# Kernel tuning notes

Hardware: AMD Instinct MI355X
Metric: run time of the kernel (lower is better)

## Reference

```python
import jax, jax.numpy as jnp
import numpy as np

V = 50000   # vocab
E = 512     # embedding_dim
H = 512     # hidden_dim
HD = 256    # hidden per direction = H // 2
L = 2       # num_layers
B = 64      # batch
T = 256     # sequence_length
K = 7       # tagset size
START, STOP = 5, 6
NEG = -10000.0


def setup_inputs() -> dict:
    key = jax.random.key(0)
    ks = jax.random.split(key, 12)
    sentence = jax.random.randint(ks[0], (T, B), 0, V)          # [T, B] token ids
    emb = jax.random.normal(ks[1], (V, E), jnp.float32) * 0.02  # embedding table
    # PyTorch LSTM params, stacked: [layer, direction, ...]; gate order i,f,g,o
    w_ih = jax.random.normal(ks[2], (L, 2, 4 * HD, E), jnp.float32) * 0.05
    w_hh = jax.random.normal(ks[3], (L, 2, 4 * HD, HD), jnp.float32) * 0.05
    b_ih = jax.random.normal(ks[4], (L, 2, 4 * HD), jnp.float32) * 0.05
    b_hh = jax.random.normal(ks[5], (L, 2, 4 * HD), jnp.float32) * 0.05
    w_out = jax.random.normal(ks[6], (K, H), jnp.float32) * 0.05  # hidden2tag
    b_out = jax.random.normal(ks[7], (K,), jnp.float32) * 0.05
    trans = jax.random.normal(ks[8], (K, K), jnp.float32)
    trans = trans.at[START, :].set(NEG).at[:, STOP].set(NEG)      # CRF transitions[next, prev]
    h0 = jax.random.normal(ks[9], (2 * L, B, HD), jnp.float32)    # random init hidden, as in module
    c0 = jax.random.normal(ks[10], (2 * L, B, HD), jnp.float32)
    return dict(sentence=sentence, emb=emb, w_ih=w_ih, w_hh=w_hh, b_ih=b_ih,
                b_hh=b_hh, w_out=w_out, b_out=b_out, trans=trans, h0=h0, c0=c0)


def _lstm_dir(x, w_ih_d, w_hh_d, b_ih_d, b_hh_d, h0_d, c0_d, reverse):
    # x: [T, B, in]; returns hidden sequence [T, B, HD]
    xg = jnp.einsum('tbe,ge->tbg', x, w_ih_d) + b_ih_d + b_hh_d  # precompute input gates

    def step(carry, g_t):
        h, c = carry
        g = g_t + h @ w_hh_d.T
        i, f, gg, o = jnp.split(g, 4, axis=-1)
        i = jax.nn.sigmoid(i); f = jax.nn.sigmoid(f)
        gg = jnp.tanh(gg);     o = jax.nn.sigmoid(o)
        c = f * c + i * gg
        h = o * jnp.tanh(c)
        return (h, c), h

    _, hs = jax.lax.scan(step, (h0_d, c0_d), xg, reverse=reverse)
    return hs


def _bilstm_feats(sentence, emb, w_ih, w_hh, b_ih, b_hh, w_out, b_out, h0, c0):
    x = emb[sentence]  # [T, B, E]
    for l in range(L):
        hf = _lstm_dir(x, w_ih[l, 0], w_hh[l, 0], b_ih[l, 0], b_hh[l, 0], h0[2 * l], c0[2 * l], False)
        hb = _lstm_dir(x, w_ih[l, 1], w_hh[l, 1], b_ih[l, 1], b_hh[l, 1], h0[2 * l + 1], c0[2 * l + 1], True)
        x = jnp.concatenate([hf, hb], axis=-1)  # [T, B, H]
    return x @ w_out.T + b_out  # [T, B, K]


def _viterbi(feats, trans):
    # feats: [T, B, K]; vectorized over batch (original looped per sequence)
    v0 = jnp.full((B, K), NEG, feats.dtype).at[:, START].set(0.0)

    def step(v, feat_t):
        sc = v[:, None, :] + trans[None, :, :]   # [B, next, prev]
        bp = jnp.argmax(sc, axis=2)              # [B, K]
        v2 = jnp.max(sc, axis=2) + feat_t
        return v2, bp

    v, bps = jax.lax.scan(step, v0, feats)       # bps: [T, B, K]
    term = v + trans[STOP][None, :]
    last = jnp.argmax(term, axis=1)              # [B]
    score = jnp.max(term, axis=1)                # [B] path score

    def back(tag, bp_t):
        prev = jnp.take_along_axis(bp_t, tag[:, None], axis=1)[:, 0]
        return prev, tag

    _, path = jax.lax.scan(back, last, bps, reverse=True)  # [T, B]
    return path.T.astype(jnp.int32), score


def reference(sentence, emb, w_ih, w_hh, b_ih, b_hh, w_out, b_out, trans, h0, c0):
    feats = _bilstm_feats(sentence, emb, w_ih, w_hh, b_ih, b_hh, w_out, b_out, h0, c0)
    best_path, path_score = _viterbi(feats, trans)
    return best_path, path_score
```

## Files before the change

kernel.cpp:

```cpp
#include <hip/hip_runtime.h>
#include <stdint.h>

#define T_LEN 256
#define BATCH 64
#define EDIM  512
#define HDIM  256
#define GDIM  1024
#define KTAG  7
#define NEGV  -10000.0f

using u16 = unsigned short;
using u32 = unsigned int;
using u64 = unsigned long long;

typedef short    bf16x8 __attribute__((ext_vector_type(8)));
typedef float    f32x4  __attribute__((ext_vector_type(4)));

__device__ __forceinline__ float bflo(u32 u) { return __uint_as_float(u << 16); }
__device__ __forceinline__ float bfhi(u32 u) { return __uint_as_float(u & 0xffff0000u); }
__device__ __forceinline__ float bf2f(u16 u) { return __uint_as_float(((u32)u) << 16); }
__device__ __forceinline__ u16 f2bf(float f) {
    u32 x = __float_as_uint(f);
    u32 r = x + 0x7fffu + ((x >> 16) & 1u);
    return (u16)(r >> 16);
}
__device__ __forceinline__ u32 pack2(float a, float b) {
    return (u32)f2bf(a) | ((u32)f2bf(b) << 16);
}
__device__ __forceinline__ float fsig(float x)  { return __builtin_amdgcn_rcpf(1.f + __expf(-x)); }
__device__ __forceinline__ float ftanh(float x) { return 1.f - 2.f * __builtin_amdgcn_rcpf(1.f + __expf(2.f * x)); }

__device__ __forceinline__ int dot4i8(int a, int b, int c) {
#if __has_builtin(__builtin_amdgcn_sdot4)
    return __builtin_amdgcn_sdot4(a, b, c, false);
#else
    c += (int)(signed char)(a & 0xff)         * (int)(signed char)(b & 0xff);
    c += (int)(signed char)((a >> 8) & 0xff)  * (int)(signed char)((b >> 8) & 0xff);
    c += (int)(signed char)((a >> 16) & 0xff) * (int)(signed char)((b >> 16) & 0xff);
    c += (int)(signed char)(a >> 24)          * (int)(signed char)(b >> 24);
    return c;
#endif
}

__device__ __forceinline__ void bar_lds() {
    asm volatile("s_waitcnt lgkmcnt(0)" ::: "memory");
    __builtin_amdgcn_s_barrier();
    asm volatile("" ::: "memory");
}

__device__ __forceinline__ void gload_lds16(const void* g, void* l) {
    __builtin_amdgcn_global_load_lds((const __attribute__((address_space(1))) u32*)g,
                                     (__attribute__((address_space(3))) u32*)l, 16, 0, 0);
}

__global__ __launch_bounds__(64) void embed_k(const int* __restrict__ sent,
                                              const float* __restrict__ emb,
                                              u16* __restrict__ X) {
    int tb = blockIdx.x;
    int tok = sent[tb];
    const float4* src = (const float4*)(emb + (size_t)tok * EDIM);
    float4 a = src[threadIdx.x * 2];
    float4 b = src[threadIdx.x * 2 + 1];
    uint4 o;
    o.x = pack2(a.x, a.y); o.y = pack2(a.z, a.w);
    o.z = pack2(b.x, b.y); o.w = pack2(b.z, b.w);
    ((uint4*)(X + (size_t)tb * EDIM))[threadIdx.x] = o;
}

__global__ __launch_bounds__(256) void conv_wih(const float* __restrict__ W,
                                                u16* __restrict__ WB) {
    int g = blockIdx.x * 256 + threadIdx.x;
    const float4* src = (const float4*)(W + (size_t)g * 8);
    float4 a = src[0], b = src[1];
    uint4 o;
    o.x = pack2(a.x, a.y); o.y = pack2(a.z, a.w);
    o.z = pack2(b.x, b.y); o.w = pack2(b.z, b.w);
    *(uint4*)(WB + (size_t)g * 8) = o;
}

__global__ __launch_bounds__(256) void repack_whh_i8(const float* __restrict__ Whh,
                                                     uint4* __restrict__ WQ,
                                                     float* __restrict__ SCL) {
    int g  = blockIdx.x * 256 + threadIdx.x;
    int ld = g >> 10, row = g & 1023;
    const float* src = Whh + ((size_t)ld * GDIM + row) * HDIM;
    float m = 1e-30f;
    for (int k4 = 0; k4 < 64; ++k4) {
        float4 w = ((const float4*)src)[k4];
        m = fmaxf(m, fmaxf(fmaxf(fabsf(w.x), fabsf(w.y)), fmaxf(fabsf(w.z), fabsf(w.w))));
    }
    float inv = 127.f / m;
    SCL[ld * GDIM + row] = m / 127.f;
    int r = row >> 8, j = row & 255;
    for (int c8 = 0; c8 < 16; ++c8) {
        u32 dw[4];
        #pragma unroll
        for (int d4 = 0; d4 < 4; ++d4) {
            u32 p = 0;
            #pragma unroll
            for (int bb = 0; bb < 4; ++bb) {
                float w = src[c8 * 16 + d4 * 4 + bb];
                int q = (int)rintf(w * inv);
                q = q > 127 ? 127 : (q < -127 ? -127 : q);
                p |= ((u32)(q & 0xff)) << (8 * bb);
            }
            dw[d4] = p;
        }
        WQ[(size_t)(((ld * 4 + r) * 16 + c8) * 256 + j)] =
            (uint4){dw[0], dw[1], dw[2], dw[3]};
    }
}

__global__ __launch_bounds__(256) void gemm_xg(const u16* __restrict__ A,
                                               const u16* __restrict__ W,
                                               const float* __restrict__ Bih,
                                               const float* __restrict__ Bhh,
                                               u16* __restrict__ XG) {
    const int d    = blockIdx.z;
    const int brow = blockIdx.x;
    const int bcol = blockIdx.y;
    const int tid  = threadIdx.x;
    const int lane = tid & 63;
    const int wv   = tid >> 6;
    const int l15  = lane & 15;
    const int quad = lane >> 4;
    const int wr   = wv >> 1, wc = wv & 1;

    __shared__ u16 As[128 * 64];
    __shared__ u16 Bs[128 * 64];

    const u16* Wd = W + (size_t)d * GDIM * EDIM;
    const int srow = tid >> 3;
    const int scol = (tid & 7) * 8;
    const u16* ga = A  + (size_t)(brow * 128 + srow) * EDIM + scol;
    const u16* gb = Wd + (size_t)(bcol * 128 + srow) * EDIM + scol;
    u16* la = As + srow * 64 + scol;
    u16* lb = Bs + srow * 64 + scol;

    f32x4 acc[4][4];
    #pragma unroll
    for (int mt = 0; mt < 4; ++mt)
        #pragma unroll
        for (int nt = 0; nt < 4; ++nt)
            acc[mt][nt] = (f32x4){0.f, 0.f, 0.f, 0.f};

    for (int k0 = 0; k0 < EDIM; k0 += 64) {
        #pragma unroll
        for (int it = 0; it < 4; ++it) {
            gload_lds16(ga + (size_t)(it * 32) * EDIM + k0, la + it * 32 * 64);
            gload_lds16(gb + (size_t)(it * 32) * EDIM + k0, lb + it * 32 * 64);
        }
        __syncthreads();
        #pragma unroll
        for (int ks = 0; ks < 2; ++ks) {
            bf16x8 av[4], bv[4];
            #pragma unroll
            for (int mt = 0; mt < 4; ++mt)
                av[mt] = *(const bf16x8*)(As + (wr * 64 + mt * 16 + l15) * 64 + ks * 32 + quad * 8);
            #pragma unroll
            for (int nt = 0; nt < 4; ++nt)
                bv[nt] = *(const bf16x8*)(Bs + (wc * 64 + nt * 16 + l15) * 64 + ks * 32 + quad * 8);
            #pragma unroll
            for (int mt = 0; mt < 4; ++mt)
                #pragma unroll
                for (int nt = 0; nt < 4; ++nt)
                    acc[mt][nt] = __builtin_amdgcn_mfma_f32_16x16x32_bf16(av[mt], bv[nt], acc[mt][nt], 0, 0, 0);
        }
        __syncthreads();
    }

    u16* xgd = XG + (size_t)d * ((size_t)16384 * GDIM);
    #pragma unroll
    for (int nt = 0; nt < 4; ++nt) {
        int col = bcol * 128 + wc * 64 + nt * 16 + l15;
        float bias = Bih[d * GDIM + col] + Bhh[d * GDIM + col];
        #pragma unroll
        for (int mt = 0; mt < 4; ++mt) {
            int row0 = brow * 128 + wr * 64 + mt * 16 + quad * 4;
            #pragma unroll
            for (int r = 0; r < 4; ++r)
                xgd[(size_t)(row0 + r) * GDIM + col] = f2bf(acc[mt][nt][r] + bias);
        }
    }
}

__global__ __launch_bounds__(1024) void lstm_scan_i8(
        const u16* __restrict__ XG,
        const uint4* __restrict__ WQ,
        const float* __restrict__ SCL,
        const float* __restrict__ H0,
        const float* __restrict__ C0,
        u16* __restrict__ XOUT) {
    const int b   = blockIdx.x & 63;
    const int d   = blockIdx.x >> 6;
    const int tid = threadIdx.x;
    const int j   = tid & 255;
    const int q   = tid >> 8;

    __shared__ uint4  hq[2][16];
    __shared__ float4 psv[4 * 256];

    uint4 Wr[4][4];
    #pragma unroll
    for (int r = 0; r < 4; ++r)
        #pragma unroll
        for (int c = 0; c < 4; ++c)
            Wr[r][c] = WQ[(size_t)(((d * 4 + r) * 16 + q * 4 + c) * 256 + j)];

    float scl0 = 0.f, scl1 = 0.f, scl2 = 0.f, scl3 = 0.f, cst = 0.f;
    if (q == 0) {
        scl0 = SCL[d * GDIM + 0 * 256 + j];
        scl1 = SCL[d * GDIM + 1 * 256 + j];
        scl2 = SCL[d * GDIM + 2 * 256 + j];
        scl3 = SCL[d * GDIM + 3 * 256 + j];
        float h0v = H0[((size_t)d * BATCH + b) * HDIM + j];
        cst       = C0[((size_t)d * BATCH + b) * HDIM + j];
        int qz = (int)rintf(h0v * 31.75f);
        qz = qz > 127 ? 127 : (qz < -127 ? -127 : qz);
        ((signed char*)hq)[j] = (signed char)qz;
    }
    __syncthreads();

    const u16* xgp = XG + (size_t)d * ((size_t)16384 * GDIM) + (size_t)b * GDIM + j;
    u16 xe[4], xo[4];
    if (q == 0) {
        int t0 = d ? T_LEN - 1 : 0;
        int t1 = d ? T_LEN - 2 : 1;
        #pragma unroll
        for (int r = 0; r < 4; ++r) xe[r] = xgp[(size_t)t0 * (BATCH * GDIM) + r * 256];
        #pragma unroll
        for (int r = 0; r < 4; ++r) xo[r] = xgp[(size_t)t1 * (BATCH * GDIM) + r * 256];
    }

    float hs = 4.f / 127.f;

#define SCAN_SUBSTEP(S, XA, RB, WB)                                                     \
    {                                                                                   \
        const int t_ = d ? (T_LEN - 1 - (S)) : (S);                                     \
        const uint4* hb = (const uint4*)hq + (RB) * 16 + q * 4;                         \
        uint4 hv[4];                                                                    \
        _Pragma("unroll")                                                               \
        for (int c = 0; c < 4; ++c) hv[c] = hb[c];          \
        int a0 = 0, a1 = 0, a2 = 0, a3 = 0;                                             \
        _Pragma("unroll")                                                               \
        for (int c = 0; c < 4; ++c) {                                                   \
            a0 = dot4i8(Wr[0][c].x, hv[c].x, a0);                                       \
            a0 = dot4i8(Wr[0][c].y, hv[c].y, a0);                                       \
            a0 = dot4i8(Wr[0][c].z, hv[c].z, a0);                                       \
            a0 = dot4i8(Wr[0][c].w, hv[c].w, a0);                                       \
            a1 = dot4i8(Wr[1][c].x, hv[c].x, a1);                                       \
            a1 = dot4i8(Wr[1][c].y, hv[c].y, a1);                                       \
            a1 = dot4i8(Wr[1][c].z, hv[c].z, a1);                                       \
            a1 = dot4i8(Wr[1][c].w, hv[c].w, a1);                                       \
            a2 = dot4i8(Wr[2][c].x, hv[c].x, a2);                                       \
            a2 = dot4i8(Wr[2][c].y, hv[c].y, a2);                                       \
            a2 = dot4i8(Wr[2][c].z, hv[c].z, a2);                                       \
            a2 = dot4i8(Wr[2][c].w, hv[c].w, a2);                                       \
            a3 = dot4i8(Wr[3][c].x, hv[c].x, a3);                                       \
            a3 = dot4i8(Wr[3][c].y, hv[c].y, a3);                                       \
            a3 = dot4i8(Wr[3][c].z, hv[c].z, a3);                                       \
            a3 = dot4i8(Wr[3][c].w, hv[c].w, a3);                                       \
        }                                                                               \
             \
        psv[q * 256 + j] = (float4){(float)a0, (float)a1, (float)a2, (float)a3};        \
        bar_lds();                                                                      \
        if (q == 0) {                                                                   \
            float4 p0 = psv[j], p1 = psv[256 + j], p2 = psv[512 + j], p3 = psv[768 + j];\
            float g0 = bf2f(XA[0]) + (p0.x + p1.x + p2.x + p3.x) * (scl0 * hs);         \
            float g1 = bf2f(XA[1]) + (p0.y + p1.y + p2.y + p3.y) * (scl1 * hs);         \
            float g2 = bf2f(XA[2]) + (p0.z + p1.z + p2.z + p3.z) * (scl2 * hs);         \
            float g3 = bf2f(XA[3]) + (p0.w + p1.w + p2.w + p3.w) * (scl3 * hs);         \
            float iv = fsig(g0), fv = fsig(g1), gv = ftanh(g2), ov = fsig(g3);          \
            cst = fv * cst + iv * gv;                                                   \
            float h = ov * ftanh(cst);                                                  \
            XOUT[((size_t)t_ * BATCH + b) * EDIM + d * HDIM + j] = f2bf(h);             \
            int qz = (int)rintf(h * 127.f);                     \
            qz = qz > 127 ? 127 : (qz < -127 ? -127 : qz);                              \
            ((signed char*)hq)[(WB) * 256 + j] = (signed char)qz;                       \
            int s2 = ((S) + 2 < T_LEN) ? (S) + 2 : T_LEN - 1;                           \
            int t2 = d ? (T_LEN - 1 - s2) : s2;                                         \
            _Pragma("unroll")                                                           \
            for (int r = 0; r < 4; ++r)                                                 \
                XA[r] = xgp[(size_t)t2 * (BATCH * GDIM) + r * 256];                     \
        }                                                                               \
        bar_lds();                                                                      \
        hs = 1.f / 127.f;                                                               \
    }

    for (int s = 0; s < T_LEN; s += 2) {
        SCAN_SUBSTEP(s,     xe, 0, 1);
        SCAN_SUBSTEP(s + 1, xo, 1, 0);
    }
#undef SCAN_SUBSTEP
}

__global__ __launch_bounds__(64) void feats_k(const u16* __restrict__ X,
                                              const float* __restrict__ Wout,
                                              const float* __restrict__ Bout,
                                              float* __restrict__ F) {
    int tb = blockIdx.x, lane = threadIdx.x;
    uint4 xv = ((const uint4*)(X + (size_t)tb * EDIM))[lane];
    float xf[8];
    xf[0] = bflo(xv.x); xf[1] = bfhi(xv.x); xf[2] = bflo(xv.y); xf[3] = bfhi(xv.y);
    xf[4] = bflo(xv.z); xf[5] = bfhi(xv.z); xf[6] = bflo(xv.w); xf[7] = bfhi(xv.w);
    #pragma unroll
    for (int k = 0; k < KTAG; ++k) {
        const float4* wpo = (const float4*)(Wout + (size_t)k * EDIM) + lane * 2;
        float4 wa = wpo[0], wb = wpo[1];
        float p = 0.0f;
        p = fmaf(xf[0], wa.x, p); p = fmaf(xf[1], wa.y, p);
        p = fmaf(xf[2], wa.z, p); p = fmaf(xf[3], wa.w, p);
        p = fmaf(xf[4], wb.x, p); p = fmaf(xf[5], wb.y, p);
        p = fmaf(xf[6], wb.z, p); p = fmaf(xf[7], wb.w, p);
        #pragma unroll
        for (int off = 32; off > 0; off >>= 1) p += __shfl_xor(p, off, 64);
        if (lane == 0) F[tb * 8 + k] = p + Bout[k];
    }
}

__global__ __launch_bounds__(64) void viterbi_k(const float* __restrict__ F,
                                                const float* __restrict__ Trans,
                                                u64* __restrict__ BP8,
                                                float* __restrict__ OUT) {
    int b = threadIdx.x;
    float tr[KTAG][KTAG];
    #pragma unroll
    for (int n = 0; n < KTAG; ++n)
        #pragma unroll
        for (int p = 0; p < KTAG; ++p)
            tr[n][p] = Trans[n * KTAG + p];

    float v[KTAG];
    #pragma unroll
    for (int k = 0; k < KTAG; ++k) v[k] = (k == 5) ? 0.0f : NEGV;

    float cf[KTAG], nf[KTAG];
    #pragma unroll
    for (int n = 0; n < KTAG; ++n) cf[n] = F[b * 8 + n];

    for (int t = 0; t < T_LEN; ++t) {
        int tp = (t + 1 < T_LEN) ? t + 1 : t;
        #pragma unroll
        for (int n = 0; n < KTAG; ++n) nf[n] = F[((tp)*BATCH + b) * 8 + n];

        u64 pk = 0;
        float nv[KTAG];
        #pragma unroll
        for (int n = 0; n < KTAG; ++n) {
            float best = v[0] + tr[n][0]; int bi = 0;
            #pragma unroll
            for (int p = 1; p < KTAG; ++p) {
                float s = v[p] + tr[n][p];
                if (s > best) { best = s; bi = p; }
            }
            pk |= ((u64)bi) << (8 * n);
            nv[n] = best + cf[n];
        }
        BP8[t * BATCH + b] = pk;
        #pragma unroll
        for (int n = 0; n < KTAG; ++n) { v[n] = nv[n]; cf[n] = nf[n]; }
    }
    float bs = v[0] + tr[6][0]; int tag = 0;
    #pragma unroll
    for (int k = 1; k < KTAG; ++k) {
        float s = v[k] + tr[6][k];
        if (s > bs) { bs = s; tag = k; }
    }
    OUT[T_LEN * BATCH + b] = bs;
    for (int t = T_LEN - 1; t >= 0; --t) {
        OUT[(size_t)b * T_LEN + t] = (float)tag;
        tag = (int)((BP8[t * BATCH + b] >> (8 * tag)) & 0xff);
    }
}

extern "C" void kernel_launch(void* const* d_in, const int* in_sizes, int n_in,
                              void* d_out, int out_size, void* d_ws, size_t ws_size,
                              hipStream_t stream) {
    const int*   sent  = (const int*)d_in[0];
    const float* emb   = (const float*)d_in[1];
    const float* w_ih  = (const float*)d_in[2];
    const float* w_hh  = (const float*)d_in[3];
    const float* b_ih  = (const float*)d_in[4];
    const float* b_hh  = (const float*)d_in[5];
    const float* w_out = (const float*)d_in[6];
    const float* b_out = (const float*)d_in[7];
    const float* trans = (const float*)d_in[8];
    const float* h0    = (const float*)d_in[9];
    const float* c0    = (const float*)d_in[10];
    float* out = (float*)d_out;

    char* ws = (char*)d_ws;
    u16*   xg    = (u16*)(ws);
    u16*   x     = (u16*)(ws + 67108864);
    u16*   wihB  = (u16*)(ws + 83886080);
    uint4* wq    = (uint4*)(ws + 88080384);
    float* scl   = (float*)(ws + 89128960);
    float* feats = (float*)(ws + 89145344);
    u64*   bp8   = (u64*)(ws + 89669632);

    embed_k<<<16384, 64, 0, stream>>>(sent, emb, x);
    conv_wih<<<1024, 256, 0, stream>>>(w_ih, wihB);
    repack_whh_i8<<<16, 256, 0, stream>>>(w_hh, wq, scl);

    for (int l = 0; l < 2; ++l) {
        gemm_xg<<<dim3(128, 8, 2), 256, 0, stream>>>(
            x, wihB + (size_t)l * 2 * GDIM * EDIM,
            b_ih + (size_t)l * 2 * GDIM, b_hh + (size_t)l * 2 * GDIM, xg);
        lstm_scan_i8<<<128, 1024, 0, stream>>>(
            xg, wq + (size_t)l * 32768, scl + (size_t)l * 2048,
            h0 + (size_t)l * 2 * BATCH * HDIM, c0 + (size_t)l * 2 * BATCH * HDIM, x);
    }

    feats_k<<<16384, 64, 0, stream>>>(x, w_out, b_out, feats);
    viterbi_k<<<1, 64, 0, stream>>>(feats, trans, bp8, out);
}
```

Baseline: 951.4 us.

## Double-buffer LDS tiles in input-gate GEMM and pin scan occupancy

The input-gate GEMM now keeps two LDS buffers per operand, so the next K-tile's global loads overlap the MFMA work on the current tile, and it removes one barrier per iteration. It also requests two blocks per CU. The LSTM scan kernel gets an amdgpu_waves_per_eu(4,4) attribute that caps register use at a fixed occupancy. Extra LDS use and register limits may cause spills or lower occupancy. The scan kernel most likely dominates total time, so the GEMM change may matter little.

```diff
diff --git a/kernel.cpp b/kernel.cpp
--- a/kernel.cpp
+++ b/kernel.cpp
@@ -111,11 +111,11 @@
     }
 }
 
-__global__ __launch_bounds__(256) void gemm_xg(const u16* __restrict__ A,
-                                               const u16* __restrict__ W,
-                                               const float* __restrict__ Bih,
-                                               const float* __restrict__ Bhh,
-                                               u16* __restrict__ XG) {
+__global__ __launch_bounds__(256, 2) void gemm_xg(const u16* __restrict__ A,
+                                                  const u16* __restrict__ W,
+                                                  const float* __restrict__ Bih,
+                                                  const float* __restrict__ Bhh,
+                                                  u16* __restrict__ XG) {
     const int d    = blockIdx.z;
     const int brow = blockIdx.x;
     const int bcol = blockIdx.y;
@@ -126,16 +126,15 @@
     const int quad = lane >> 4;
     const int wr   = wv >> 1, wc = wv & 1;
 
-    __shared__ u16 As[128 * 64];
-    __shared__ u16 Bs[128 * 64];
+    __shared__ u16 As[2][128 * 64];
+    __shared__ u16 Bs[2][128 * 64];
 
     const u16* Wd = W + (size_t)d * GDIM * EDIM;
     const int srow = tid >> 3;
     const int scol = (tid & 7) * 8;
     const u16* ga = A  + (size_t)(brow * 128 + srow) * EDIM + scol;
     const u16* gb = Wd + (size_t)(bcol * 128 + srow) * EDIM + scol;
-    u16* la = As + srow * 64 + scol;
-    u16* lb = Bs + srow * 64 + scol;
+    const int loff = srow * 64 + scol;
 
     f32x4 acc[4][4];
     #pragma unroll
@@ -144,22 +143,34 @@
         for (int nt = 0; nt < 4; ++nt)
             acc[mt][nt] = (f32x4){0.f, 0.f, 0.f, 0.f};
 
-    for (int k0 = 0; k0 < EDIM; k0 += 64) {
-        #pragma unroll
-        for (int it = 0; it < 4; ++it) {
-            gload_lds16(ga + (size_t)(it * 32) * EDIM + k0, la + it * 32 * 64);
-            gload_lds16(gb + (size_t)(it * 32) * EDIM + k0, lb + it * 32 * 64);
+    #pragma unroll
+    for (int it = 0; it < 4; ++it) {
+        gload_lds16(ga + (size_t)(it * 32) * EDIM, &As[0][loff + it * 32 * 64]);
+        gload_lds16(gb + (size_t)(it * 32) * EDIM, &Bs[0][loff + it * 32 * 64]);
+    }
+    __syncthreads();
+
+    int cur = 0;
+    for (int t = 0; t < 8; ++t) {
+        if (t < 7) {
+            int k0 = (t + 1) * 64;
+            #pragma unroll
+            for (int it = 0; it < 4; ++it) {
+                gload_lds16(ga + (size_t)(it * 32) * EDIM + k0, &As[cur ^ 1][loff + it * 32 * 64]);
+                gload_lds16(gb + (size_t)(it * 32) * EDIM + k0, &Bs[cur ^ 1][loff + it * 32 * 64]);
+            }
         }
-        __syncthreads();
+        const u16* Ab = As[cur];
+        const u16* Bb = Bs[cur];
         #pragma unroll
         for (int ks = 0; ks < 2; ++ks) {
             bf16x8 av[4], bv[4];
             #pragma unroll
             for (int mt = 0; mt < 4; ++mt)
-                av[mt] = *(const bf16x8*)(As + (wr * 64 + mt * 16 + l15) * 64 + ks * 32 + quad * 8);
+                av[mt] = *(const bf16x8*)(Ab + (wr * 64 + mt * 16 + l15) * 64 + ks * 32 + quad * 8);
             #pragma unroll
             for (int nt = 0; nt < 4; ++nt)
-                bv[nt] = *(const bf16x8*)(Bs + (wc * 64 + nt * 16 + l15) * 64 + ks * 32 + quad * 8);
+                bv[nt] = *(const bf16x8*)(Bb + (wc * 64 + nt * 16 + l15) * 64 + ks * 32 + quad * 8);
             #pragma unroll
             for (int mt = 0; mt < 4; ++mt)
                 #pragma unroll
@@ -167,6 +178,7 @@
                     acc[mt][nt] = __builtin_amdgcn_mfma_f32_16x16x32_bf16(av[mt], bv[nt], acc[mt][nt], 0, 0, 0);
         }
         __syncthreads();
+        cur ^= 1;
     }
 
     u16* xgd = XG + (size_t)d * ((size_t)16384 * GDIM);
@@ -184,7 +196,8 @@
     }
 }
 
-__global__ __launch_bounds__(1024) void lstm_scan_i8(
+__global__ __attribute__((amdgpu_waves_per_eu(4, 4))) __launch_bounds__(1024)
+void lstm_scan_i8(
         const u16* __restrict__ XG,
         const uint4* __restrict__ WQ,
         const float* __restrict__ SCL,
```

After: 936.1 us. Within noise of the previous version (-1.6%).
